# Optimization experiments

Hardware: AMD Instinct MI355X
Metric: run time of the kernel (lower is better)

## Reference

```python
import jax, jax.numpy as jnp
import numpy as np

D_IN, D_HIDDEN, DT_RANK = 768, 16, 48


def setup_inputs() -> dict:
    key = jax.random.key(0)
    ks = jax.random.split(key, 6)
    b, l, d, n, r = 2, 2048, D_IN, D_HIDDEN, DT_RANK
    p = 3 * n + 2 * d + 2 * r  # x_proj output width = 1680
    x = jax.random.normal(ks[0], (b, l, d), jnp.float32)
    z = jax.random.normal(ks[1], (b, d, l), jnp.float32)
    # A_log = log(repeat(arange(1, n+1), 'n -> d n'))
    A_log = jnp.log(jnp.broadcast_to(jnp.arange(1, n + 1, dtype=jnp.float32), (d, n)))
    D = jnp.ones((d,), jnp.float32)
    W_xproj = jax.random.normal(ks[2], (p, d), jnp.float32) / np.sqrt(d)
    W_dt = jax.random.normal(ks[3], (d, r), jnp.float32) / np.sqrt(r)
    # dt bias init: inverse-softplus of dt ~ LogUniform(1e-3, 1e-1)
    dt = jnp.exp(jax.random.uniform(ks[4], (d,)) * (np.log(0.1) - np.log(0.001)) + np.log(0.001))
    dt = jnp.clip(dt, 1e-4)
    b_dt = dt + jnp.log(-jnp.expm1(-dt))
    return dict(x=x, z=z, A_log=A_log, D=D, W_xproj=W_xproj, W_dt=W_dt, b_dt=b_dt)


def reference(x, z, A_log, D, W_xproj, W_dt, b_dt):
    b, l, d = x.shape
    n = A_log.shape[1]
    r = W_dt.shape[1]
    A = -jnp.exp(A_log)                      # (d, n)
    proj = x @ W_xproj.T                     # (b, l, 3n + 2d + 2r)
    Bm = proj[..., :n]                       # (b, l, n)  input matrix B
    Cm = proj[..., 2 * n:3 * n]              # (b, l, n)  output matrix C
    dt = proj[..., 3 * n + 2 * d:3 * n + 2 * d + r]   # (b, l, r)
    # NOTE: source adds dt_proj bias via the Linear AND again via delta_bias -> 2*b_dt
    delta = jax.nn.softplus(dt @ W_dt.T + 2.0 * b_dt)  # (b, l, d)
    dA = jnp.exp(delta[..., None] * A)                  # (b, l, d, n)
    dBu = (delta * x)[..., None] * Bm[:, :, None, :]    # (b, l, d, n)

    def step(h, inp):
        dA_t, dBu_t, C_t = inp
        h = dA_t * h + dBu_t                 # (b, d, n)
        return h, jnp.einsum('bdn,bn->bd', h, C_t)

    h0 = jnp.zeros((b, d, n), x.dtype)
    _, ys = jax.lax.scan(step, h0, (jnp.swapaxes(dA, 0, 1), jnp.swapaxes(dBu, 0, 1), jnp.swapaxes(Cm, 0, 1)))
    y = jnp.swapaxes(ys, 0, 1) + x * D       # (b, l, d)  + skip D*u
    zl = jnp.swapaxes(z, 1, 2)               # z is (b, d, l) -> (b, l, d)
    return y * (zl * jax.nn.sigmoid(zl))     # gate with silu(z)
```

## Files before the change

kernel.cpp:

```cpp
#include <hip/hip_runtime.h>
#include <math.h>

#define BATCH 2
#define LSEQ  2048
#define DIM   768
#define NST   16
#define RDT   48
#define BL    (BATCH*LSEQ)
#define NCHUNK 32
#define CLEN   (LSEQ/NCHUNK)
#define CPAD   68
#define NPACK  (CLEN/4)
#define LP4    (LSEQ/4)
#define L2E    1.4426950408889634f

typedef __attribute__((ext_vector_type(8))) short short8;
typedef __attribute__((ext_vector_type(4))) float float4e;

__device__ __forceinline__ ushort f2bf(float f) {
    union { float f; unsigned u; } v; v.f = f;
    unsigned u = v.u;
    u += 0x7fffu + ((u >> 16) & 1u);
    return (ushort)(u >> 16);
}
__device__ __forceinline__ unsigned pk2bf(float a, float b) {
    return (unsigned)f2bf(a) | ((unsigned)f2bf(b) << 16);
}

__global__ __launch_bounds__(256) void pack_kernel(
        const float* __restrict__ x, const float* __restrict__ Wx,
        ushort* __restrict__ xbf, float* __restrict__ xT,
        ushort* __restrict__ Wbf) {
    if (blockIdx.y == 12) {
        const int blk = blockIdx.z * 32 + blockIdx.x;
        for (int idx = blk * 256 + threadIdx.x; idx < 80 * DIM; idx += 64 * 256) {
            const int j = idx / DIM;
            const int k = idx - j * DIM;
            const int row = (j < 16) ? j : ((j < 32) ? (j + 16) : (j + 1552));
            Wbf[idx] = f2bf(Wx[(size_t)row * DIM + k]);
        }
        return;
    }
    __shared__ float tile[64 * 68];
    const int r0 = blockIdx.x * 64;
    const int c0 = blockIdx.y * 64;
    const int b  = blockIdx.z;
    const int tid = threadIdx.x;
    const int c4 = tid & 15;
    const int rb = tid >> 4;
    #pragma unroll
    for (int rr = 0; rr < 4; ++rr) {
        const int row = rr * 16 + rb;
        const size_t gbase = ((size_t)b * LSEQ + (r0 + row)) * DIM + c0;
        const float4 v = *(const float4*)(x + gbase + c4 * 4);
        *(float4*)&tile[row * 68 + c4 * 4] = v;
        const uint2 bf = make_uint2(pk2bf(v.x, v.y), pk2bf(v.z, v.w));
        *(uint2*)(xbf + gbase + c4 * 4) = bf;
    }
    __syncthreads();
    const int c  = tid & 63;
    const int l0 = (tid >> 6) * 16;
    float* dst = xT + ((size_t)b * DIM + c0 + c) * LSEQ + r0 + l0;
    #pragma unroll
    for (int q = 0; q < 4; ++q) {
        const float4 v = make_float4(tile[(l0 + 4*q + 0) * 68 + c],
                                     tile[(l0 + 4*q + 1) * 68 + c],
                                     tile[(l0 + 4*q + 2) * 68 + c],
                                     tile[(l0 + 4*q + 3) * 68 + c]);
        *(float4*)(dst + 4 * q) = v;
    }
}

__global__ __launch_bounds__(64) void proj_gemm_kernel(
        const ushort* __restrict__ xbf, const ushort* __restrict__ Wbf,
        float* __restrict__ Bpk, float* __restrict__ Cpk,
        float* __restrict__ dtpT) {
    const int m0   = blockIdx.x * 16;
    const int lane = threadIdx.x;
    const int col  = lane & 15;
    const int quad = lane >> 4;

    const short* A  = (const short*)xbf + (size_t)(m0 + col) * DIM + quad * 8;
    const short* Bw = (const short*)Wbf;

    float4e acc[5] = {};
    #pragma unroll 6
    for (int kk = 0; kk < 24; ++kk) {
        const short8 a = *(const short8*)(A + kk * 32);
        #pragma unroll
        for (int nt = 0; nt < 5; ++nt) {
            const short8 bf = *(const short8*)(Bw + (size_t)(nt * 16 + col) * DIM + kk * 32 + quad * 8);
            acc[nt] = __builtin_amdgcn_mfma_f32_16x16x32_bf16(a, bf, acc[nt], 0, 0, 0);
        }
    }

    const int b  = m0 >> 11;
    const int t0 = m0 & 2047;
    const size_t pk4 = ((size_t)(b * LP4 + (t0 >> 2) + quad)) * NST + col;
    ((float4*)Bpk)[pk4] = *(float4*)&acc[0];
    ((float4*)Cpk)[pk4] = *(float4*)&acc[1];
    #pragma unroll
    for (int nt = 2; nt < 5; ++nt) {
        const int r = (nt - 2) * 16 + col;
        *(float4*)(dtpT + ((size_t)(b * RDT + r)) * LSEQ + t0 + quad * 4) = *(float4*)&acc[nt];
    }
}

__global__ __launch_bounds__(256) void xpose_kernel(
        const float* __restrict__ in, float* __restrict__ out, int R, int C) {
    __shared__ float tile[64 * 68];
    const int r0 = blockIdx.x * 64;
    const int c0 = blockIdx.y * 64;
    const int b  = blockIdx.z;
    const int tid = threadIdx.x;
    const int c4 = tid & 15;
    const int rb = tid >> 4;
    #pragma unroll
    for (int rr = 0; rr < 4; ++rr) {
        const int row = rr * 16 + rb;
        const float4 v = *(const float4*)(in + ((size_t)b * R + (r0 + row)) * C + c0 + c4 * 4);
        *(float4*)&tile[row * 68 + c4 * 4] = v;
    }
    __syncthreads();
    const int c  = tid & 63;
    const int l0 = (tid >> 6) * 16;
    float* dst = out + ((size_t)b * C + (c0 + c)) * R + r0 + l0;
    #pragma unroll
    for (int q = 0; q < 4; ++q) {
        const float4 v = make_float4(tile[(l0 + 4*q + 0) * 68 + c],
                                     tile[(l0 + 4*q + 1) * 68 + c],
                                     tile[(l0 + 4*q + 2) * 68 + c],
                                     tile[(l0 + 4*q + 3) * 68 + c]);
        *(float4*)(dst + 4 * q) = v;
    }
}

__global__ __launch_bounds__(512) void scan_kernel(
        const float* __restrict__ xT, const float* __restrict__ z,
        const float* __restrict__ A_log, const float* __restrict__ Dp,
        const float* __restrict__ Bpk, const float* __restrict__ Cpk,
        const float* __restrict__ dtpT, const float* __restrict__ Wdt,
        const float* __restrict__ bdt, float* __restrict__ yT) {
    __shared__ float sdel[NCHUNK * CPAD];
    __shared__ float sdlx[NCHUNK * CPAD];
    __shared__ float sx[NCHUNK * CPAD];
    __shared__ float sP[NCHUNK][NST];
    __shared__ float sq[NCHUNK][NST];
    __shared__ float sw[RDT];

    const int tid = threadIdx.x;
    const int ch = blockIdx.x;
    const int b = ch / DIM;
    const int d = ch % DIM;
    const size_t row = (size_t)ch * LSEQ;

    if (tid < RDT) sw[tid] = Wdt[(size_t)d * RDT + tid];
    const float4 xv4 = ((const float4*)(xT + row))[tid];
    ((float4*)sx)[(tid >> 4) * (CPAD / 4) + (tid & 15)] = xv4;
    __syncthreads();

    {
        const float bb = 2.0f * bdt[d];
        const float* dbase = dtpT + (size_t)b * RDT * LSEQ;
        float4 acc = make_float4(bb, bb, bb, bb);
        #pragma unroll 3
        for (int k4 = 0; k4 < RDT / 4; ++k4) {
            const float4 wv = ((const float4*)sw)[k4];
            #pragma unroll
            for (int j = 0; j < 4; ++j) {
                const int k = k4 * 4 + j;
                const float wk = (j == 0) ? wv.x : (j == 1) ? wv.y : (j == 2) ? wv.z : wv.w;
                const float4 v = ((const float4*)(dbase + (size_t)k * LSEQ))[tid];
                acc.x = fmaf(v.x, wk, acc.x);
                acc.y = fmaf(v.y, wk, acc.y);
                acc.z = fmaf(v.z, wk, acc.z);
                acc.w = fmaf(v.w, wk, acc.w);
            }
        }
        float4 sp;
        sp.x = (acc.x > 20.f) ? acc.x : __logf(1.f + __expf(acc.x));
        sp.y = (acc.y > 20.f) ? acc.y : __logf(1.f + __expf(acc.y));
        sp.z = (acc.z > 20.f) ? acc.z : __logf(1.f + __expf(acc.z));
        sp.w = (acc.w > 20.f) ? acc.w : __logf(1.f + __expf(acc.w));
        const int sidx = (tid >> 4) * (CPAD / 4) + (tid & 15);
        ((float4*)sdel)[sidx] = sp;
        ((float4*)sdlx)[sidx] = make_float4(sp.x * xv4.x, sp.y * xv4.y,
                                            sp.z * xv4.z, sp.w * xv4.w);
    }
    __syncthreads();

    const int g = tid >> 4;
    const int n = tid & 15;
    const float Aln2 = -__expf(A_log[d * NST + n]) * L2E;
    const float4* Bg = (const float4*)Bpk + ((size_t)(b * LP4 + g * NPACK) * NST + n);
    const float4* Cg = (const float4*)Cpk + ((size_t)(b * LP4 + g * NPACK) * NST + n);
    const float* dchunk  = sdel + g * CPAD;
    const float* uxchunk = sdlx + g * CPAD;

    {
        float h = 0.f, Ptot = 1.f;
        float4 Bn_ = Bg[0];
        #pragma unroll 4
        for (int p = 0; p < NPACK; ++p) {
            const float4 B4 = Bn_;
            if (p < NPACK - 1) Bn_ = Bg[(p + 1) * NST];
            const float4 dl = *(const float4*)(dchunk + 4 * p);
            const float4 ux = *(const float4*)(uxchunk + 4 * p);
            const float u0 = ux.x * B4.x, u1 = ux.y * B4.y;
            const float u2 = ux.z * B4.z, u3 = ux.w * B4.w;
            const float e0  = __builtin_amdgcn_exp2f(Aln2 * dl.x);
            const float dA1 = __builtin_amdgcn_exp2f(Aln2 * dl.y);
            const float dA2 = __builtin_amdgcn_exp2f(Aln2 * dl.z);
            const float dA3 = __builtin_amdgcn_exp2f(Aln2 * dl.w);
            float s = u0;
            s = fmaf(dA1, s, u1); s = fmaf(dA2, s, u2); s = fmaf(dA3, s, u3);
            const float E3 = ((e0 * dA1) * (dA2 * dA3));
            h = fmaf(E3, h, s);
            Ptot *= E3;
        }
        sP[g][n] = Ptot;
        sq[g][n] = h;
    }
    __syncthreads();

    {
        float Pc = sP[g][n], qc = sq[g][n];
        #pragma unroll
        for (int s = 1; s < NCHUNK; s <<= 1) {
            float Pp = 1.f, qp = 0.f;
            if (g >= s) { Pp = sP[g - s][n]; qp = sq[g - s][n]; }
            __syncthreads();
            qc = fmaf(Pc, qp, qc);
            Pc *= Pp;
            sP[g][n] = Pc; sq[g][n] = qc;
            __syncthreads();
        }
    }

    {
        float h = (g == 0) ? 0.f : sq[g - 1][n];
        float* ybuf = sdel;
        float4 Bn_ = Bg[0];
        float4 Cn_ = Cg[0];
        #pragma unroll 4
        for (int p = 0; p < NPACK; ++p) {
            const float4 B4 = Bn_, C4 = Cn_;
            if (p < NPACK - 1) { Bn_ = Bg[(p + 1) * NST]; Cn_ = Cg[(p + 1) * NST]; }
            const float4 dl = *(const float4*)(dchunk + 4 * p);
            const float4 ux = *(const float4*)(uxchunk + 4 * p);
            const float u0 = ux.x * B4.x, u1 = ux.y * B4.y;
            const float u2 = ux.z * B4.z, u3 = ux.w * B4.w;
            const float E0  = __builtin_amdgcn_exp2f(Aln2 * dl.x);
            const float dA1 = __builtin_amdgcn_exp2f(Aln2 * dl.y);
            const float dA2 = __builtin_amdgcn_exp2f(Aln2 * dl.z);
            const float dA3 = __builtin_amdgcn_exp2f(Aln2 * dl.w);
            const float E1 = E0 * dA1, E2 = E1 * dA2, E3 = E2 * dA3;
            const float s0 = u0;
            const float s1 = fmaf(dA1, s0, u1);
            const float s2 = fmaf(dA2, s1, u2);
            const float s3 = fmaf(dA3, s2, u3);
            const float h0 = fmaf(E0, h, s0);
            const float h1 = fmaf(E1, h, s1);
            const float h2 = fmaf(E2, h, s2);
            const float h3 = fmaf(E3, h, s3);
            h = h3;
            float p0 = h0 * C4.x, p1 = h1 * C4.y, p2 = h2 * C4.z, p3 = h3 * C4.w;
            p0 += __shfl_xor(p0, 1); p0 += __shfl_xor(p0, 2);
            p1 += __shfl_xor(p1, 1); p1 += __shfl_xor(p1, 2);
            p2 += __shfl_xor(p2, 1); p2 += __shfl_xor(p2, 2);
            p3 += __shfl_xor(p3, 1); p3 += __shfl_xor(p3, 2);
            float v = (n & 1) ? ((n & 2) ? p3 : p1) : ((n & 2) ? p2 : p0);
            v += __shfl_xor(v, 4);
            v += __shfl_xor(v, 8);
            if (n < 4) ybuf[g * CPAD + 4 * p + n] = v;
        }
    }
    __syncthreads();

    {
        const float Dd = Dp[d];
        const float* zrow = z + row;
        float* yrow = yT + row;
        #pragma unroll
        for (int i = tid; i < LSEQ; i += 512) {
            const int idx = (i >> 6) * CPAD + (i & 63);
            const float zv = zrow[i];
            const float sig = 1.0f / (1.0f + __expf(-zv));
            yrow[i] = fmaf(sx[idx], Dd, sdel[idx]) * zv * sig;
        }
    }
}

extern "C" void kernel_launch(void* const* d_in, const int* in_sizes, int n_in,
                              void* d_out, int out_size, void* d_ws, size_t ws_size,
                              hipStream_t stream) {
    const float* x     = (const float*)d_in[0];
    const float* z     = (const float*)d_in[1];
    const float* A_log = (const float*)d_in[2];
    const float* D     = (const float*)d_in[3];
    const float* Wx    = (const float*)d_in[4];
    const float* Wdt   = (const float*)d_in[5];
    const float* bdt   = (const float*)d_in[6];
    float* out = (float*)d_out;

    float* ws    = (float*)d_ws;
    float* Bpk   = ws;
    float* Cpk   = Bpk + (size_t)BATCH * LP4 * NST * 4;
    float* dtpT  = Cpk + (size_t)BATCH * LP4 * NST * 4;
    float* xT    = dtpT + (size_t)BATCH * RDT * LSEQ;
    float* yT    = xT;
    ushort* xbf  = (ushort*)(xT + (size_t)BATCH * DIM * LSEQ);
    ushort* Wbf  = xbf + (size_t)BATCH * LSEQ * DIM;

    hipLaunchKernelGGL(pack_kernel, dim3(LSEQ / 64, DIM / 64 + 1, BATCH), dim3(256), 0, stream,
                       x, Wx, xbf, xT, Wbf);
    hipLaunchKernelGGL(proj_gemm_kernel, dim3(BL / 16), dim3(64), 0, stream,
                       xbf, Wbf, Bpk, Cpk, dtpT);
    hipLaunchKernelGGL(scan_kernel, dim3(BATCH * DIM), dim3(512), 0, stream,
                       xT, z, A_log, D, Bpk, Cpk, dtpT, Wdt, bdt, yT);
    hipLaunchKernelGGL(xpose_kernel, dim3(DIM / 64, LSEQ / 64, BATCH), dim3(256), 0, stream,
                       yT, out, DIM, LSEQ);
}
```

Before: 156.2 us.

## Drop bf16 copy of x, convert in GEMM; use DPP reductions and vectorized epilogue

The pack kernel no longer writes a bf16 copy of x. The projection GEMM now reads fp32 x directly and converts it to bf16 in registers, which removes one global write and re-read of x but doubles the bytes the GEMM loads for its A operand. Both transposes change to a 65-padded shared tile with scalar transposed stores and row reads. The scan's shuffle reductions become DPP row operations, and its gating epilogue is vectorized to float4, one element group per thread.

New measurement: 156.6 us. No clear change (+0.2%).

```diff
diff --git a/kernel.cpp b/kernel.cpp
--- a/kernel.cpp
+++ b/kernel.cpp
@@ -23,15 +23,18 @@
     u += 0x7fffu + ((u >> 16) & 1u);
     return (ushort)(u >> 16);
 }
-__device__ __forceinline__ unsigned pk2bf(float a, float b) {
-    return (unsigned)f2bf(a) | ((unsigned)f2bf(b) << 16);
+
+template <int CTRL>
+__device__ __forceinline__ float dpp_add(float v) {
+    const int s = __builtin_amdgcn_update_dpp(__float_as_int(v), __float_as_int(v),
+                                              CTRL, 0xF, 0xF, false);
+    return v + __int_as_float(s);
 }
 
 __global__ __launch_bounds__(256) void pack_kernel(
         const float* __restrict__ x, const float* __restrict__ Wx,
-        ushort* __restrict__ xbf, float* __restrict__ xT,
-        ushort* __restrict__ Wbf) {
-    if (blockIdx.y == 12) {
+        float* __restrict__ xT, ushort* __restrict__ Wbf) {
+    if (blockIdx.y == DIM / 64) {
         const int blk = blockIdx.z * 32 + blockIdx.x;
         for (int idx = blk * 256 + threadIdx.x; idx < 80 * DIM; idx += 64 * 256) {
             const int j = idx / DIM;
@@ -41,38 +44,41 @@
         }
         return;
     }
-    __shared__ float tile[64 * 68];
+    __shared__ float tile[64 * 65];
     const int r0 = blockIdx.x * 64;
     const int c0 = blockIdx.y * 64;
     const int b  = blockIdx.z;
     const int tid = threadIdx.x;
-    const int c4 = tid & 15;
-    const int rb = tid >> 4;
-    #pragma unroll
-    for (int rr = 0; rr < 4; ++rr) {
-        const int row = rr * 16 + rb;
-        const size_t gbase = ((size_t)b * LSEQ + (r0 + row)) * DIM + c0;
-        const float4 v = *(const float4*)(x + gbase + c4 * 4);
-        *(float4*)&tile[row * 68 + c4 * 4] = v;
-        const uint2 bf = make_uint2(pk2bf(v.x, v.y), pk2bf(v.z, v.w));
-        *(uint2*)(xbf + gbase + c4 * 4) = bf;
-    }
-    __syncthreads();
-    const int c  = tid & 63;
-    const int l0 = (tid >> 6) * 16;
-    float* dst = xT + ((size_t)b * DIM + c0 + c) * LSEQ + r0 + l0;
-    #pragma unroll
-    for (int q = 0; q < 4; ++q) {
-        const float4 v = make_float4(tile[(l0 + 4*q + 0) * 68 + c],
-                                     tile[(l0 + 4*q + 1) * 68 + c],
-                                     tile[(l0 + 4*q + 2) * 68 + c],
-                                     tile[(l0 + 4*q + 3) * 68 + c]);
-        *(float4*)(dst + 4 * q) = v;
+    {
+        const int c4 = tid & 15, rb = tid >> 4;
+        #pragma unroll
+        for (int rr = 0; rr < 4; ++rr) {
+            const int row = rr * 16 + rb;
+            const float4 v = *(const float4*)(x + ((size_t)b * LSEQ + r0 + row) * DIM + c0 + c4 * 4);
+            tile[(c4 * 4 + 0) * 65 + row] = v.x;
+            tile[(c4 * 4 + 1) * 65 + row] = v.y;
+            tile[(c4 * 4 + 2) * 65 + row] = v.z;
+            tile[(c4 * 4 + 3) * 65 + row] = v.w;
+        }
+    }
+    __syncthreads();
+    {
+        const int t4 = tid & 15, dq = tid >> 4;
+        #pragma unroll
+        for (int pass = 0; pass < 4; ++pass) {
+            const int dd = pass * 16 + dq;
+            float4 v;
+            v.x = tile[dd * 65 + t4 * 4 + 0];
+            v.y = tile[dd * 65 + t4 * 4 + 1];
+            v.z = tile[dd * 65 + t4 * 4 + 2];
+            v.w = tile[dd * 65 + t4 * 4 + 3];
+            *(float4*)(xT + ((size_t)b * DIM + c0 + dd) * LSEQ + r0 + t4 * 4) = v;
+        }
     }
 }
 
 __global__ __launch_bounds__(64) void proj_gemm_kernel(
-        const ushort* __restrict__ xbf, const ushort* __restrict__ Wbf,
+        const float* __restrict__ x, const ushort* __restrict__ Wbf,
         float* __restrict__ Bpk, float* __restrict__ Cpk,
         float* __restrict__ dtpT) {
     const int m0   = blockIdx.x * 16;
@@ -80,13 +86,19 @@
     const int col  = lane & 15;
     const int quad = lane >> 4;
 
-    const short* A  = (const short*)xbf + (size_t)(m0 + col) * DIM + quad * 8;
+    const float* A  = x + (size_t)(m0 + col) * DIM + quad * 8;
     const short* Bw = (const short*)Wbf;
 
     float4e acc[5] = {};
-    #pragma unroll 6
+    #pragma unroll 4
     for (int kk = 0; kk < 24; ++kk) {
-        const short8 a = *(const short8*)(A + kk * 32);
+        const float4 a0 = *(const float4*)(A + kk * 32);
+        const float4 a1 = *(const float4*)(A + kk * 32 + 4);
+        short8 a;
+        a[0] = (short)f2bf(a0.x); a[1] = (short)f2bf(a0.y);
+        a[2] = (short)f2bf(a0.z); a[3] = (short)f2bf(a0.w);
+        a[4] = (short)f2bf(a1.x); a[5] = (short)f2bf(a1.y);
+        a[6] = (short)f2bf(a1.z); a[7] = (short)f2bf(a1.w);
         #pragma unroll
         for (int nt = 0; nt < 5; ++nt) {
             const short8 bf = *(const short8*)(Bw + (size_t)(nt * 16 + col) * DIM + kk * 32 + quad * 8);
@@ -108,30 +120,36 @@
 
 __global__ __launch_bounds__(256) void xpose_kernel(
         const float* __restrict__ in, float* __restrict__ out, int R, int C) {
-    __shared__ float tile[64 * 68];
+    __shared__ float tile[64 * 65];
     const int r0 = blockIdx.x * 64;
     const int c0 = blockIdx.y * 64;
     const int b  = blockIdx.z;
     const int tid = threadIdx.x;
-    const int c4 = tid & 15;
-    const int rb = tid >> 4;
-    #pragma unroll
-    for (int rr = 0; rr < 4; ++rr) {
-        const int row = rr * 16 + rb;
-        const float4 v = *(const float4*)(in + ((size_t)b * R + (r0 + row)) * C + c0 + c4 * 4);
-        *(float4*)&tile[row * 68 + c4 * 4] = v;
-    }
-    __syncthreads();
-    const int c  = tid & 63;
-    const int l0 = (tid >> 6) * 16;
-    float* dst = out + ((size_t)b * C + (c0 + c)) * R + r0 + l0;
-    #pragma unroll
-    for (int q = 0; q < 4; ++q) {
-        const float4 v = make_float4(tile[(l0 + 4*q + 0) * 68 + c],
-                                     tile[(l0 + 4*q + 1) * 68 + c],
-                                     tile[(l0 + 4*q + 2) * 68 + c],
-                                     tile[(l0 + 4*q + 3) * 68 + c]);
-        *(float4*)(dst + 4 * q) = v;
+    {
+        const int c4 = tid & 15, rb = tid >> 4;
+        #pragma unroll
+        for (int rr = 0; rr < 4; ++rr) {
+            const int row = rr * 16 + rb;
+            const float4 v = *(const float4*)(in + ((size_t)b * R + r0 + row) * C + c0 + c4 * 4);
+            tile[(c4 * 4 + 0) * 65 + row] = v.x;
+            tile[(c4 * 4 + 1) * 65 + row] = v.y;
+            tile[(c4 * 4 + 2) * 65 + row] = v.z;
+            tile[(c4 * 4 + 3) * 65 + row] = v.w;
+        }
+    }
+    __syncthreads();
+    {
+        const int t4 = tid & 15, dq = tid >> 4;
+        #pragma unroll
+        for (int pass = 0; pass < 4; ++pass) {
+            const int dd = pass * 16 + dq;
+            float4 v;
+            v.x = tile[dd * 65 + t4 * 4 + 0];
+            v.y = tile[dd * 65 + t4 * 4 + 1];
+            v.z = tile[dd * 65 + t4 * 4 + 2];
+            v.w = tile[dd * 65 + t4 * 4 + 3];
+            *(float4*)(out + ((size_t)b * C + c0 + dd) * R + r0 + t4 * 4) = v;
+        }
     }
 }
 
@@ -265,13 +283,13 @@
             const float h3 = fmaf(E3, h, s3);
             h = h3;
             float p0 = h0 * C4.x, p1 = h1 * C4.y, p2 = h2 * C4.z, p3 = h3 * C4.w;
-            p0 += __shfl_xor(p0, 1); p0 += __shfl_xor(p0, 2);
-            p1 += __shfl_xor(p1, 1); p1 += __shfl_xor(p1, 2);
-            p2 += __shfl_xor(p2, 1); p2 += __shfl_xor(p2, 2);
-            p3 += __shfl_xor(p3, 1); p3 += __shfl_xor(p3, 2);
+            p0 = dpp_add<0xB1>(p0); p0 = dpp_add<0x4E>(p0);
+            p1 = dpp_add<0xB1>(p1); p1 = dpp_add<0x4E>(p1);
+            p2 = dpp_add<0xB1>(p2); p2 = dpp_add<0x4E>(p2);
+            p3 = dpp_add<0xB1>(p3); p3 = dpp_add<0x4E>(p3);
             float v = (n & 1) ? ((n & 2) ? p3 : p1) : ((n & 2) ? p2 : p0);
-            v += __shfl_xor(v, 4);
-            v += __shfl_xor(v, 8);
+            v = dpp_add<0x124>(v);
+            v = dpp_add<0x128>(v);
             if (n < 4) ybuf[g * CPAD + 4 * p + n] = v;
         }
     }
@@ -281,13 +299,17 @@
         const float Dd = Dp[d];
         const float* zrow = z + row;
         float* yrow = yT + row;
-        #pragma unroll
-        for (int i = tid; i < LSEQ; i += 512) {
-            const int idx = (i >> 6) * CPAD + (i & 63);
-            const float zv = zrow[i];
-            const float sig = 1.0f / (1.0f + __expf(-zv));
-            yrow[i] = fmaf(sx[idx], Dd, sdel[idx]) * zv * sig;
-        }
+        const int t = tid * 4;
+        const int idx = (t >> 6) * CPAD + (t & 63);
+        const float4 yv = *(const float4*)(sdel + idx);
+        const float4 xv = *(const float4*)(sx + idx);
+        const float4 zv = ((const float4*)zrow)[tid];
+        float4 o;
+        o.x = fmaf(xv.x, Dd, yv.x) * zv.x / (1.f + __expf(-zv.x));
+        o.y = fmaf(xv.y, Dd, yv.y) * zv.y / (1.f + __expf(-zv.y));
+        o.z = fmaf(xv.z, Dd, yv.z) * zv.z / (1.f + __expf(-zv.z));
+        o.w = fmaf(xv.w, Dd, yv.w) * zv.w / (1.f + __expf(-zv.w));
+        ((float4*)yrow)[tid] = o;
     }
 }
 
@@ -309,13 +331,12 @@
     float* dtpT  = Cpk + (size_t)BATCH * LP4 * NST * 4;
     float* xT    = dtpT + (size_t)BATCH * RDT * LSEQ;
     float* yT    = xT;
-    ushort* xbf  = (ushort*)(xT + (size_t)BATCH * DIM * LSEQ);
-    ushort* Wbf  = xbf + (size_t)BATCH * LSEQ * DIM;
+    ushort* Wbf  = (ushort*)(xT + (size_t)BATCH * DIM * LSEQ);
 
     hipLaunchKernelGGL(pack_kernel, dim3(LSEQ / 64, DIM / 64 + 1, BATCH), dim3(256), 0, stream,
-                       x, Wx, xbf, xT, Wbf);
+                       x, Wx, xT, Wbf);
     hipLaunchKernelGGL(proj_gemm_kernel, dim3(BL / 16), dim3(64), 0, stream,
-                       xbf, Wbf, Bpk, Cpk, dtpT);
+                       x, Wbf, Bpk, Cpk, dtpT);
     hipLaunchKernelGGL(scan_kernel, dim3(BATCH * DIM), dim3(512), 0, stream,
                        xT, z, A_log, D, Bpk, Cpk, dtpT, Wdt, bdt, yT);
     hipLaunchKernelGGL(xpose_kernel, dim3(DIM / 64, LSEQ / 64, BATCH), dim3(256), 0, stream,
```
